# Performance work log

Measured on AMD Instinct MI355X. Metric: run time of the kernel, lower is better.

The kernel has to match this reference:

```python
import jax, jax.numpy as jnp
import numpy as np

N = 20000   # nodes
K = 32      # neighbors per node (kNN graph)
C = 128     # input feature dim
H = 256     # h_theta hidden/output dim
E = N * K   # edges


def setup_inputs() -> dict:
    key = jax.random.key(0)
    k1, k2, k3, k4 = jax.random.split(key, 4)
    node_features = jax.random.normal(k1, (N, C), dtype=jnp.float32)
    senders = jax.random.randint(k2, (E,), 0, N)              # neighbor node per edge
    receivers = jnp.repeat(jnp.arange(N), K)                  # center node per edge (k-NN: exactly K each)
    W1 = jax.random.normal(k3, (2 * C, H), dtype=jnp.float32) * (1.0 / np.sqrt(2 * C))
    b1 = jnp.zeros((H,), dtype=jnp.float32)
    W2 = jax.random.normal(k4, (H, H), dtype=jnp.float32) * (1.0 / np.sqrt(H))
    b2 = jnp.zeros((H,), dtype=jnp.float32)
    return {"node_features": node_features, "senders": senders, "receivers": receivers,
            "W1": W1, "b1": b1, "W2": W2, "b2": b2}


def reference(node_features, senders, receivers, W1, b1, W2, b2):
    # gather: x_v (center) and x_vp (neighbor) per edge -> [E, C]
    x_v = node_features[receivers]
    x_vp = node_features[senders]
    # edge feature: concat([x_v, x_vp - x_v]) -> [E, 2C]
    e = jnp.concatenate([x_v, x_vp - x_v], axis=-1)
    # h_theta MLP per edge -> [E, H]
    h = jnp.dot(jax.nn.relu(jnp.dot(e, W1) + b1), W2) + b2
    # max-reduce over each node's incident edges -> [N, H]
    return jax.ops.segment_max(h, receivers, num_segments=N)
```

## Files before the change

### kernel.cpp

```cpp
#include <hip/hip_runtime.h>
#include <hip/hip_bf16.h>

#define NN    20000
#define KNN   32
#define CIN   128
#define HD    256
#define EE    (NN * KNN)
#define NT    10
#define NBLK  (NN / (2 * NT))

typedef __bf16 bf16x8_t __attribute__((ext_vector_type(8)));
typedef __bf16 bf16x4_t __attribute__((ext_vector_type(4)));
typedef float  f32x4_t  __attribute__((ext_vector_type(4)));

__global__ void ec_prep(const float* __restrict__ nf, const float* __restrict__ W1,
                        const float* __restrict__ W2, __bf16* __restrict__ nfb,
                        __bf16* __restrict__ w1g, __bf16* __restrict__ w2t) {
    int bid = blockIdx.x;
    if (bid < (NN * CIN) / 1024) {
        int i = (bid * 256 + threadIdx.x) * 4;
        float4 v = *(const float4*)(nf + i);
        bf16x4_t b = { (__bf16)v.x, (__bf16)v.y, (__bf16)v.z, (__bf16)v.w };
        *(bf16x4_t*)(nfb + i) = b;
    } else {
        int idx = (bid - (NN * CIN) / 1024) * 256 + threadIdx.x;
        int k = idx >> 8, n = idx & 255;
        float v = (k < CIN) ? (W1[k * 256 + n] - W1[(k + CIN) * 256 + n])
                            : W1[k * 256 + n];
        int kt = k >> 5, qr = (k >> 3) & 3, j = k & 7;
        w1g[(size_t)((kt * 4 + qr) * 256 + n) * 8 + j] = (__bf16)v;
        w2t[n * 256 + k] = (__bf16)W2[k * 256 + n];
    }
}

__global__ __launch_bounds__(512, 1) void ec_pz(
    const __bf16* __restrict__ nfb, const __bf16* __restrict__ w1g,
    const float* __restrict__ b1, float* __restrict__ Pq, __bf16* __restrict__ Zq)
{
    __shared__ __attribute__((aligned(16))) float ldsT[32 * 256];

    const int tid  = threadIdx.x;
    const int lane = tid & 63;
    const int wave = tid >> 6;
    const int qrow = lane >> 4;
    const int lcol = lane & 15;
    const int blk  = blockIdx.x;
    const int fsl  = wave * 32;

    bf16x8_t xv[2][4];
#pragma unroll
    for (int ni = 0; ni < 2; ++ni) {
        const __bf16* row = nfb + (size_t)(blk * 32 + ni * 16 + lcol) * CIN;
#pragma unroll
        for (int c = 0; c < 4; ++c)
            xv[ni][c] = *(const bf16x8_t*)(row + c * 32 + qrow * 8);
    }

    float4 bias1[2];
#pragma unroll
    for (int mi = 0; mi < 2; ++mi)
        bias1[mi] = *(const float4*)(b1 + fsl + mi * 16 + qrow * 4);

    {
        f32x4_t ay[2][2];
#pragma unroll
        for (int mi = 0; mi < 2; ++mi)
#pragma unroll
            for (int ni = 0; ni < 2; ++ni)
                ay[mi][ni] = (f32x4_t){0.f, 0.f, 0.f, 0.f};
#pragma unroll
        for (int kt = 0; kt < 4; ++kt) {
            bf16x8_t wy[2];
#pragma unroll
            for (int mi = 0; mi < 2; ++mi)
                wy[mi] = *(const bf16x8_t*)(w1g +
                    (size_t)((kt * 4 + qrow) * 256 + fsl + mi * 16 + lcol) * 8);
#pragma unroll
            for (int mi = 0; mi < 2; ++mi)
#pragma unroll
                for (int ni = 0; ni < 2; ++ni)
                    ay[mi][ni] = __builtin_amdgcn_mfma_f32_16x16x32_bf16(
                        wy[mi], xv[ni][kt], ay[mi][ni], 0, 0, 0);
        }
#pragma unroll
        for (int mi = 0; mi < 2; ++mi)
#pragma unroll
            for (int ni = 0; ni < 2; ++ni) {
                f32x4_t v = ay[mi][ni];
                v[0] += bias1[mi].x; v[1] += bias1[mi].y;
                v[2] += bias1[mi].z; v[3] += bias1[mi].w;
                *(f32x4_t*)(ldsT + (ni * 16 + lcol) * 256 + fsl + mi * 16 + qrow * 4) = v;
            }
    }
    __syncthreads();
    {
        float4* dst = (float4*)(Pq + (size_t)blk * 32 * 256);
        const float4* src = (const float4*)ldsT;
#pragma unroll
        for (int i = 0; i < 4; ++i)
            dst[tid * 4 + i] = src[tid * 4 + i];
    }
    __syncthreads();

    {
        f32x4_t az[2][2];
#pragma unroll
        for (int mi = 0; mi < 2; ++mi)
#pragma unroll
            for (int ni = 0; ni < 2; ++ni)
                az[mi][ni] = (f32x4_t){0.f, 0.f, 0.f, 0.f};
#pragma unroll
        for (int kt = 0; kt < 4; ++kt) {
            bf16x8_t wy[2];
#pragma unroll
            for (int mi = 0; mi < 2; ++mi)
                wy[mi] = *(const bf16x8_t*)(w1g +
                    (size_t)((16 + kt * 4 + qrow) * 256 + fsl + mi * 16 + lcol) * 8);
#pragma unroll
            for (int mi = 0; mi < 2; ++mi)
#pragma unroll
                for (int ni = 0; ni < 2; ++ni)
                    az[mi][ni] = __builtin_amdgcn_mfma_f32_16x16x32_bf16(
                        wy[mi], xv[ni][kt], az[mi][ni], 0, 0, 0);
        }
#pragma unroll
        for (int mi = 0; mi < 2; ++mi)
#pragma unroll
            for (int ni = 0; ni < 2; ++ni)
                *(f32x4_t*)(ldsT + (ni * 16 + lcol) * 256 + fsl + mi * 16 + qrow * 4)
                    = az[mi][ni];
    }
    __syncthreads();
    {
        const float4* src = (const float4*)ldsT;
        __bf16* dst = Zq + (size_t)blk * 32 * 256;
#pragma unroll
        for (int i = 0; i < 4; ++i) {
            float4 v = src[tid * 4 + i];
            bf16x4_t b = { (__bf16)v.x, (__bf16)v.y, (__bf16)v.z, (__bf16)v.w };
            *(bf16x4_t*)(dst + (size_t)(tid * 4 + i) * 4) = b;
        }
    }
}

__global__ __launch_bounds__(512, 1) void ec_main(
    const __bf16* __restrict__ Zq,
    const int*   __restrict__ senders,
    const float* __restrict__ Pq,
    const __bf16* __restrict__ w2t,
    const float* __restrict__ b2,
    float* __restrict__ out)
{
    __shared__ __attribute__((aligned(16))) __bf16 ldsH[2][16384];
    __shared__ __attribute__((aligned(16))) float  ldsP[20 * 256];

    const int tid  = threadIdx.x;
    const int lane = tid & 63;
    const int wave = tid >> 6;
    const int qrow = lane >> 4;
    const int lcol = lane & 15;
    const int blk  = blockIdx.x;
    const int fsl  = wave * 32;
    const int fs2  = (wave >> 1) * 64;
    const int eh   = wave & 1;

    int sidxAll[NT];
#pragma unroll
    for (int tt = 0; tt < NT; ++tt)
        sidxAll[tt] = senders[(blk * NT + tt) * 64 + lane];

    {
        const float4* src = (const float4*)(Pq + (size_t)blk * 20 * 256);
        float4* dst = (float4*)ldsP;
        for (int i = tid; i < 1280; i += 512)
            dst[i] = src[i];
    }

    bf16x8_t w2f[8][4];
#pragma unroll
    for (int kt = 0; kt < 8; ++kt)
#pragma unroll
        for (int ni = 0; ni < 4; ++ni)
            w2f[kt][ni] = *(const bf16x8_t*)(w2t + (size_t)(fs2 + ni * 16 + lcol) * 256
                                                 + kt * 32 + qrow * 8);
    float bias2[4];
#pragma unroll
    for (int ni = 0; ni < 4; ++ni)
        bias2[ni] = b2[fs2 + ni * 16 + lcol];

    bf16x8_t zf[4];
#pragma unroll
    for (int c = 0; c < 4; ++c)
        zf[c] = *(const bf16x8_t*)(Zq + (size_t)sidxAll[0] * HD + fsl + c * 8);

    __syncthreads();

    {
        const int nl = 0 * 2 + (lane >> 5);
        const float* pf = ldsP + nl * 256 + fsl;
#pragma unroll
        for (int c = 0; c < 4; ++c) {
            f32x4_t p0 = *(const f32x4_t*)(pf + c * 8);
            f32x4_t p1 = *(const f32x4_t*)(pf + c * 8 + 4);
            bf16x8_t h;
#pragma unroll
            for (int j = 0; j < 4; ++j) {
                h[j]     = (__bf16)fmaxf(p0[j] + (float)zf[c][j], 0.f);
                h[j + 4] = (__bf16)fmaxf(p1[j] + (float)zf[c][j + 4], 0.f);
            }
            *(bf16x8_t*)(&ldsH[0][0] + (size_t)((wave * 4 + c) * 64 + lane) * 8) = h;
        }
    }
    __syncthreads();

#pragma unroll 1
    for (int t = 0; t < NT; ++t) {
        const int cur = t & 1;

        if (t + 1 < NT) {
#pragma unroll
            for (int c = 0; c < 4; ++c)
                zf[c] = *(const bf16x8_t*)(Zq + (size_t)sidxAll[t + 1] * HD + fsl + c * 8);
        }

        f32x4_t acc2[2][4];
#pragma unroll
        for (int mi = 0; mi < 2; ++mi)
#pragma unroll
            for (int ni = 0; ni < 4; ++ni)
                acc2[mi][ni] = (f32x4_t){0.f, 0.f, 0.f, 0.f};
#pragma unroll
        for (int kt = 0; kt < 8; ++kt) {
            bf16x8_t af[2];
#pragma unroll
            for (int mi = 0; mi < 2; ++mi)
                af[mi] = *(const bf16x8_t*)(&ldsH[cur][0] +
                    (size_t)((kt * 4 + qrow) * 64 + eh * 32 + mi * 16 + lcol) * 8);
#pragma unroll
            for (int mi = 0; mi < 2; ++mi)
#pragma unroll
                for (int ni = 0; ni < 4; ++ni)
                    acc2[mi][ni] = __builtin_amdgcn_mfma_f32_16x16x32_bf16(
                        af[mi], w2f[kt][ni], acc2[mi][ni], 0, 0, 0);
        }

#pragma unroll
        for (int ni = 0; ni < 4; ++ni) {
            float mx = -3.402823466e38f;
#pragma unroll
            for (int mi = 0; mi < 2; ++mi)
#pragma unroll
                for (int r = 0; r < 4; ++r)
                    mx = fmaxf(mx, acc2[mi][ni][r]);
            mx = fmaxf(mx, __shfl_xor(mx, 16, 64));
            mx = fmaxf(mx, __shfl_xor(mx, 32, 64));
            if (qrow == 0)
                out[(size_t)((blk * NT + t) * 2 + eh) * HD + fs2 + ni * 16 + lcol]
                    = mx + bias2[ni];
        }

        if (t + 1 < NT) {
            const int nl = (t + 1) * 2 + (lane >> 5);
            const float* pf = ldsP + nl * 256 + fsl;
#pragma unroll
            for (int c = 0; c < 4; ++c) {
                f32x4_t p0 = *(const f32x4_t*)(pf + c * 8);
                f32x4_t p1 = *(const f32x4_t*)(pf + c * 8 + 4);
                bf16x8_t h;
#pragma unroll
                for (int j = 0; j < 4; ++j) {
                    h[j]     = (__bf16)fmaxf(p0[j] + (float)zf[c][j], 0.f);
                    h[j + 4] = (__bf16)fmaxf(p1[j] + (float)zf[c][j + 4], 0.f);
                }
                *(bf16x8_t*)(&ldsH[1 - cur][0] + (size_t)((wave * 4 + c) * 64 + lane) * 8) = h;
            }
        }

        __syncthreads();
    }
}

extern "C" void kernel_launch(void* const* d_in, const int* in_sizes, int n_in,
                              void* d_out, int out_size, void* d_ws, size_t ws_size,
                              hipStream_t stream) {
    const float* nf      = (const float*)d_in[0];
    const int*   senders = (const int*)d_in[1];
    const float* W1 = (const float*)d_in[3];
    const float* b1 = (const float*)d_in[4];
    const float* W2 = (const float*)d_in[5];
    const float* b2 = (const float*)d_in[6];

    __bf16* w1g = (__bf16*)d_ws;
    __bf16* w2t = w1g + 256 * 256;
    __bf16* nfb = w2t + 256 * 256;
    __bf16* Zq  = nfb + (size_t)NN * CIN;
    float*  Pq  = (float*)(Zq + (size_t)NN * HD);

    ec_prep<<<(NN * CIN) / 1024 + 256, 256, 0, stream>>>(nf, W1, W2, nfb, w1g, w2t);
    ec_pz<<<NN / 32, 512, 0, stream>>>(nfb, w1g, b1, Pq, Zq);
    ec_main<<<NBLK, 512, 0, stream>>>(Zq, senders, Pq, w2t, b2, (float*)d_out);
}
```

Baseline: 220.9 us.

## Fold prep into projection kernel and compute hidden activations in registers

Removes the separate prep kernel. The node-feature bf16 conversion and the W1 difference/transposition now happen inside the projection kernel, which reads fp32 directly, and extra blocks transpose W2. The main kernel is restructured: each 256-thread block processes 16 nodes, and each wave owns 64 output features over all 32 edges, split into two 16-edge halves. The relu(P+Z) hidden tile is built in registers and fed straight to MFMA, replacing the LDS double-buffer and per-step barriers, and gathers are prefetched across halves. The cost is that every projection block recomputes the W1 conversion with strided fp32 loads, and the gathered Z loads are exposed with less latency hiding.

```diff
diff --git a/kernel.cpp b/kernel.cpp
--- a/kernel.cpp
+++ b/kernel.cpp
@@ -6,54 +6,50 @@
 #define CIN   128
 #define HD    256
 #define EE    (NN * KNN)
-#define NT    10
-#define NBLK  (NN / (2 * NT))
+#define NB    16
+#define NBLK  (NN / NB)
+#define PZB   (NN / 32)
 
 typedef __bf16 bf16x8_t __attribute__((ext_vector_type(8)));
 typedef __bf16 bf16x4_t __attribute__((ext_vector_type(4)));
 typedef float  f32x4_t  __attribute__((ext_vector_type(4)));
 
-__global__ void ec_prep(const float* __restrict__ nf, const float* __restrict__ W1,
-                        const float* __restrict__ W2, __bf16* __restrict__ nfb,
-                        __bf16* __restrict__ w1g, __bf16* __restrict__ w2t) {
-    int bid = blockIdx.x;
-    if (bid < (NN * CIN) / 1024) {
-        int i = (bid * 256 + threadIdx.x) * 4;
-        float4 v = *(const float4*)(nf + i);
-        bf16x4_t b = { (__bf16)v.x, (__bf16)v.y, (__bf16)v.z, (__bf16)v.w };
-        *(bf16x4_t*)(nfb + i) = b;
-    } else {
-        int idx = (bid - (NN * CIN) / 1024) * 256 + threadIdx.x;
-        int k = idx >> 8, n = idx & 255;
-        float v = (k < CIN) ? (W1[k * 256 + n] - W1[(k + CIN) * 256 + n])
-                            : W1[k * 256 + n];
-        int kt = k >> 5, qr = (k >> 3) & 3, j = k & 7;
-        w1g[(size_t)((kt * 4 + qr) * 256 + n) * 8 + j] = (__bf16)v;
-        w2t[n * 256 + k] = (__bf16)W2[k * 256 + n];
-    }
-}
-
 __global__ __launch_bounds__(512, 1) void ec_pz(
-    const __bf16* __restrict__ nfb, const __bf16* __restrict__ w1g,
-    const float* __restrict__ b1, float* __restrict__ Pq, __bf16* __restrict__ Zq)
+    const float* __restrict__ nf, const float* __restrict__ W1,
+    const float* __restrict__ W2, const float* __restrict__ b1,
+    float* __restrict__ Pq, __bf16* __restrict__ Zq, __bf16* __restrict__ w2t)
 {
     __shared__ __attribute__((aligned(16))) float ldsT[32 * 256];
 
-    const int tid  = threadIdx.x;
+    const int bid = blockIdx.x;
+    const int tid = threadIdx.x;
+
+    if (bid >= PZB) {
+        int idx = (bid - PZB) * 512 + tid;
+        int k = idx >> 8, n = idx & 255;
+        w2t[n * 256 + k] = (__bf16)W2[k * 256 + n];
+        return;
+    }
+
     const int lane = tid & 63;
     const int wave = tid >> 6;
     const int qrow = lane >> 4;
     const int lcol = lane & 15;
-    const int blk  = blockIdx.x;
     const int fsl  = wave * 32;
 
     bf16x8_t xv[2][4];
 #pragma unroll
     for (int ni = 0; ni < 2; ++ni) {
-        const __bf16* row = nfb + (size_t)(blk * 32 + ni * 16 + lcol) * CIN;
-#pragma unroll
-        for (int c = 0; c < 4; ++c)
-            xv[ni][c] = *(const bf16x8_t*)(row + c * 32 + qrow * 8);
+        const float* row = nf + (size_t)(bid * 32 + ni * 16 + lcol) * CIN;
+#pragma unroll
+        for (int c = 0; c < 4; ++c) {
+            f32x4_t a = *(const f32x4_t*)(row + c * 32 + qrow * 8);
+            f32x4_t b = *(const f32x4_t*)(row + c * 32 + qrow * 8 + 4);
+            bf16x8_t x;
+#pragma unroll
+            for (int j = 0; j < 4; ++j) { x[j] = (__bf16)a[j]; x[j + 4] = (__bf16)b[j]; }
+            xv[ni][c] = x;
+        }
     }
 
     float4 bias1[2];
@@ -70,11 +66,16 @@
                 ay[mi][ni] = (f32x4_t){0.f, 0.f, 0.f, 0.f};
 #pragma unroll
         for (int kt = 0; kt < 4; ++kt) {
+            const float* wbase = W1 + (size_t)(kt * 32 + qrow * 8) * 256;
             bf16x8_t wy[2];
 #pragma unroll
-            for (int mi = 0; mi < 2; ++mi)
-                wy[mi] = *(const bf16x8_t*)(w1g +
-                    (size_t)((kt * 4 + qrow) * 256 + fsl + mi * 16 + lcol) * 8);
+            for (int mi = 0; mi < 2; ++mi) {
+                const int col = fsl + mi * 16 + lcol;
+#pragma unroll
+                for (int j = 0; j < 8; ++j)
+                    wy[mi][j] = (__bf16)(wbase[j * 256 + col]
+                                         - wbase[(j + 128) * 256 + col]);
+            }
 #pragma unroll
             for (int mi = 0; mi < 2; ++mi)
 #pragma unroll
@@ -94,7 +95,7 @@
     }
     __syncthreads();
     {
-        float4* dst = (float4*)(Pq + (size_t)blk * 32 * 256);
+        float4* dst = (float4*)(Pq + (size_t)bid * 32 * 256);
         const float4* src = (const float4*)ldsT;
 #pragma unroll
         for (int i = 0; i < 4; ++i)
@@ -111,11 +112,15 @@
                 az[mi][ni] = (f32x4_t){0.f, 0.f, 0.f, 0.f};
 #pragma unroll
         for (int kt = 0; kt < 4; ++kt) {
+            const float* wbase = W1 + (size_t)(kt * 32 + qrow * 8 + 128) * 256;
             bf16x8_t wy[2];
 #pragma unroll
-            for (int mi = 0; mi < 2; ++mi)
-                wy[mi] = *(const bf16x8_t*)(w1g +
-                    (size_t)((16 + kt * 4 + qrow) * 256 + fsl + mi * 16 + lcol) * 8);
+            for (int mi = 0; mi < 2; ++mi) {
+                const int col = fsl + mi * 16 + lcol;
+#pragma unroll
+                for (int j = 0; j < 8; ++j)
+                    wy[mi][j] = (__bf16)wbase[j * 256 + col];
+            }
 #pragma unroll
             for (int mi = 0; mi < 2; ++mi)
 #pragma unroll
@@ -133,7 +138,7 @@
     __syncthreads();
     {
         const float4* src = (const float4*)ldsT;
-        __bf16* dst = Zq + (size_t)blk * 32 * 256;
+        __bf16* dst = Zq + (size_t)bid * 32 * 256;
 #pragma unroll
         for (int i = 0; i < 4; ++i) {
             float4 v = src[tid * 4 + i];
@@ -143,7 +148,29 @@
     }
 }
 
-__global__ __launch_bounds__(512, 1) void ec_main(
+__device__ __forceinline__ void mfma_phase(
+    const bf16x8_t (&zf)[8], const float* __restrict__ pRow, int qrow8,
+    const bf16x8_t (&w2f)[8][4], f32x4_t (&acc)[4])
+{
+#pragma unroll
+    for (int kt = 0; kt < 8; ++kt) {
+        f32x4_t p0 = *(const f32x4_t*)(pRow + kt * 32 + qrow8);
+        f32x4_t p1 = *(const f32x4_t*)(pRow + kt * 32 + qrow8 + 4);
+        bf16x8_t zz = zf[kt];
+        bf16x8_t h;
+#pragma unroll
+        for (int j = 0; j < 4; ++j) {
+            h[j]     = (__bf16)fmaxf(p0[j] + (float)zz[j],     0.f);
+            h[j + 4] = (__bf16)fmaxf(p1[j] + (float)zz[j + 4], 0.f);
+        }
+#pragma unroll
+        for (int ni = 0; ni < 4; ++ni)
+            acc[ni] = __builtin_amdgcn_mfma_f32_16x16x32_bf16(
+                h, w2f[kt][ni], acc[ni], 0, 0, 0);
+    }
+}
+
+__global__ __launch_bounds__(256, 2) void ec_main(
     const __bf16* __restrict__ Zq,
     const int*   __restrict__ senders,
     const float* __restrict__ Pq,
@@ -151,29 +178,24 @@
     const float* __restrict__ b2,
     float* __restrict__ out)
 {
-    __shared__ __attribute__((aligned(16))) __bf16 ldsH[2][16384];
-    __shared__ __attribute__((aligned(16))) float  ldsP[20 * 256];
+    __shared__ __attribute__((aligned(16))) float ldsP[NB * 256];
 
     const int tid  = threadIdx.x;
     const int lane = tid & 63;
     const int wave = tid >> 6;
     const int qrow = lane >> 4;
     const int lcol = lane & 15;
+    const int q8   = qrow * 8;
     const int blk  = blockIdx.x;
-    const int fsl  = wave * 32;
-    const int fs2  = (wave >> 1) * 64;
-    const int eh   = wave & 1;
-
-    int sidxAll[NT];
-#pragma unroll
-    for (int tt = 0; tt < NT; ++tt)
-        sidxAll[tt] = senders[(blk * NT + tt) * 64 + lane];
-
-    {
-        const float4* src = (const float4*)(Pq + (size_t)blk * 20 * 256);
+    const int fs2  = wave * 64;
+    const int n0   = blk * NB;
+
+    {
+        const float4* src = (const float4*)(Pq + (size_t)n0 * 256);
         float4* dst = (float4*)ldsP;
-        for (int i = tid; i < 1280; i += 512)
-            dst[i] = src[i];
+#pragma unroll
+        for (int i = 0; i < 4; ++i)
+            dst[tid + i * 256] = src[tid + i * 256];
     }
 
     bf16x8_t w2f[8][4];
@@ -182,101 +204,70 @@
 #pragma unroll
         for (int ni = 0; ni < 4; ++ni)
             w2f[kt][ni] = *(const bf16x8_t*)(w2t + (size_t)(fs2 + ni * 16 + lcol) * 256
-                                                 + kt * 32 + qrow * 8);
+                                                 + kt * 32 + q8);
     float bias2[4];
 #pragma unroll
     for (int ni = 0; ni < 4; ++ni)
         bias2[ni] = b2[fs2 + ni * 16 + lcol];
 
-    bf16x8_t zf[4];
-#pragma unroll
-    for (int c = 0; c < 4; ++c)
-        zf[c] = *(const bf16x8_t*)(Zq + (size_t)sidxAll[0] * HD + fsl + c * 8);
-
-    __syncthreads();
-
-    {
-        const int nl = 0 * 2 + (lane >> 5);
-        const float* pf = ldsP + nl * 256 + fsl;
-#pragma unroll
-        for (int c = 0; c < 4; ++c) {
-            f32x4_t p0 = *(const f32x4_t*)(pf + c * 8);
-            f32x4_t p1 = *(const f32x4_t*)(pf + c * 8 + 4);
-            bf16x8_t h;
-#pragma unroll
-            for (int j = 0; j < 4; ++j) {
-                h[j]     = (__bf16)fmaxf(p0[j] + (float)zf[c][j], 0.f);
-                h[j + 4] = (__bf16)fmaxf(p1[j] + (float)zf[c][j + 4], 0.f);
-            }
-            *(bf16x8_t*)(&ldsH[0][0] + (size_t)((wave * 4 + c) * 64 + lane) * 8) = h;
-        }
-    }
+    bf16x8_t zfA[8], zfB[8];
+    {
+        int sA = senders[n0 * KNN + lcol];
+        const __bf16* zb = Zq + (size_t)sA * HD + q8;
+#pragma unroll
+        for (int kt = 0; kt < 8; ++kt)
+            zfA[kt] = *(const bf16x8_t*)(zb + kt * 32);
+    }
+    int sB = senders[n0 * KNN + 16 + lcol];
+
     __syncthreads();
 
 #pragma unroll 1
-    for (int t = 0; t < NT; ++t) {
-        const int cur = t & 1;
-
-        if (t + 1 < NT) {
-#pragma unroll
-            for (int c = 0; c < 4; ++c)
-                zf[c] = *(const bf16x8_t*)(Zq + (size_t)sidxAll[t + 1] * HD + fsl + c * 8);
-        }
-
-        f32x4_t acc2[2][4];
-#pragma unroll
-        for (int mi = 0; mi < 2; ++mi)
-#pragma unroll
-            for (int ni = 0; ni < 4; ++ni)
-                acc2[mi][ni] = (f32x4_t){0.f, 0.f, 0.f, 0.f};
-#pragma unroll
-        for (int kt = 0; kt < 8; ++kt) {
-            bf16x8_t af[2];
-#pragma unroll
-            for (int mi = 0; mi < 2; ++mi)
-                af[mi] = *(const bf16x8_t*)(&ldsH[cur][0] +
-                    (size_t)((kt * 4 + qrow) * 64 + eh * 32 + mi * 16 + lcol) * 8);
-#pragma unroll
-            for (int mi = 0; mi < 2; ++mi)
-#pragma unroll
-                for (int ni = 0; ni < 4; ++ni)
-                    acc2[mi][ni] = __builtin_amdgcn_mfma_f32_16x16x32_bf16(
-                        af[mi], w2f[kt][ni], acc2[mi][ni], 0, 0, 0);
-        }
+    for (int n = 0; n < NB; ++n) {
+        const float* pRow = ldsP + n * 256;
+
+        {
+            const __bf16* zb = Zq + (size_t)sB * HD + q8;
+#pragma unroll
+            for (int kt = 0; kt < 8; ++kt)
+                zfB[kt] = *(const bf16x8_t*)(zb + kt * 32);
+        }
+        int sA2 = 0;
+        if (n + 1 < NB) sA2 = senders[(n0 + n + 1) * KNN + lcol];
+
+        f32x4_t acc[4];
+#pragma unroll
+        for (int ni = 0; ni < 4; ++ni) acc[ni] = (f32x4_t){0.f, 0.f, 0.f, 0.f};
+        mfma_phase(zfA, pRow, q8, w2f, acc);
+
+        float pm[4];
+#pragma unroll
+        for (int ni = 0; ni < 4; ++ni)
+            pm[ni] = fmaxf(fmaxf(acc[ni][0], acc[ni][1]),
+                           fmaxf(acc[ni][2], acc[ni][3]));
+
+        if (n + 1 < NB) {
+            const __bf16* zb = Zq + (size_t)sA2 * HD + q8;
+#pragma unroll
+            for (int kt = 0; kt < 8; ++kt)
+                zfA[kt] = *(const bf16x8_t*)(zb + kt * 32);
+            sB = senders[(n0 + n + 1) * KNN + 16 + lcol];
+        }
+
+#pragma unroll
+        for (int ni = 0; ni < 4; ++ni) acc[ni] = (f32x4_t){0.f, 0.f, 0.f, 0.f};
+        mfma_phase(zfB, pRow, q8, w2f, acc);
 
 #pragma unroll
         for (int ni = 0; ni < 4; ++ni) {
-            float mx = -3.402823466e38f;
-#pragma unroll
-            for (int mi = 0; mi < 2; ++mi)
-#pragma unroll
-                for (int r = 0; r < 4; ++r)
-                    mx = fmaxf(mx, acc2[mi][ni][r]);
+            float mx = fmaxf(pm[ni],
+                             fmaxf(fmaxf(acc[ni][0], acc[ni][1]),
+                                   fmaxf(acc[ni][2], acc[ni][3])));
             mx = fmaxf(mx, __shfl_xor(mx, 16, 64));
             mx = fmaxf(mx, __shfl_xor(mx, 32, 64));
             if (qrow == 0)
-                out[(size_t)((blk * NT + t) * 2 + eh) * HD + fs2 + ni * 16 + lcol]
-                    = mx + bias2[ni];
-        }
-
-        if (t + 1 < NT) {
-            const int nl = (t + 1) * 2 + (lane >> 5);
-            const float* pf = ldsP + nl * 256 + fsl;
-#pragma unroll
-            for (int c = 0; c < 4; ++c) {
-                f32x4_t p0 = *(const f32x4_t*)(pf + c * 8);
-                f32x4_t p1 = *(const f32x4_t*)(pf + c * 8 + 4);
-                bf16x8_t h;
-#pragma unroll
-                for (int j = 0; j < 4; ++j) {
-                    h[j]     = (__bf16)fmaxf(p0[j] + (float)zf[c][j], 0.f);
-                    h[j + 4] = (__bf16)fmaxf(p1[j] + (float)zf[c][j + 4], 0.f);
-                }
-                *(bf16x8_t*)(&ldsH[1 - cur][0] + (size_t)((wave * 4 + c) * 64 + lane) * 8) = h;
-            }
-        }
-
-        __syncthreads();
+                out[(size_t)(n0 + n) * HD + fs2 + ni * 16 + lcol] = mx + bias2[ni];
+        }
     }
 }
 
@@ -290,13 +281,10 @@
     const float* W2 = (const float*)d_in[5];
     const float* b2 = (const float*)d_in[6];
 
-    __bf16* w1g = (__bf16*)d_ws;
-    __bf16* w2t = w1g + 256 * 256;
-    __bf16* nfb = w2t + 256 * 256;
-    __bf16* Zq  = nfb + (size_t)NN * CIN;
+    __bf16* w2t = (__bf16*)d_ws;
+    __bf16* Zq  = w2t + 256 * 256;
     float*  Pq  = (float*)(Zq + (size_t)NN * HD);
 
-    ec_prep<<<(NN * CIN) / 1024 + 256, 256, 0, stream>>>(nf, W1, W2, nfb, w1g, w2t);
-    ec_pz<<<NN / 32, 512, 0, stream>>>(nfb, w1g, b1, Pq, Zq);
-    ec_main<<<NBLK, 512, 0, stream>>>(Zq, senders, Pq, w2t, b2, (float*)d_out);
-}
+    ec_pz<<<PZB + 128, 512, 0, stream>>>(nf, W1, W2, b1, Pq, Zq, w2t);
+    ec_main<<<NBLK, 256, 0, stream>>>(Zq, senders, Pq, w2t, b2, (float*)d_out);
+}
```

After: 617.9 us. +179.7%, slower.
